# Kernel optimization log

Hardware: AMD Instinct MI355X
Metric: run time of the kernel (lower is better)

Reference implementation:

```python
import jax, jax.numpy as jnp
import numpy as np

N, T, D, H = 32, 2048, 512, 512

def setup_inputs() -> dict:
    key = jax.random.key(0)
    k1, k2, k3, k4 = jax.random.split(key, 4)
    x = jax.random.normal(k1, (N, T, D), dtype=jnp.float32)
    h0 = jax.random.normal(k2, (N, H), dtype=jnp.float32)
    Wx = jax.random.normal(k3, (D, 4 * H), dtype=jnp.float32) / np.sqrt(D)
    Wh = jax.random.normal(k4, (H, 4 * H), dtype=jnp.float32) / np.sqrt(H)
    b = jnp.zeros((4 * H,), dtype=jnp.float32)
    return {"x": x, "h0": h0, "Wx": Wx, "Wh": Wh, "b": b}

def reference(x, h0, Wx, Wh, b):
    # Precompute input contributions for all timesteps: (N, T, 4H)
    xWx = jnp.einsum('ntd,dk->ntk', x, Wx) + b
    c0 = jnp.zeros_like(h0)
    Hd = h0.shape[-1]

    def step(carry, a_x):
        prev_h, prev_c = carry
        a = a_x + prev_h @ Wh  # (N, 4H)
        i = jax.nn.sigmoid(a[:, 0 * Hd:1 * Hd])
        f = jax.nn.sigmoid(a[:, 1 * Hd:2 * Hd])
        o = jax.nn.sigmoid(a[:, 2 * Hd:3 * Hd])
        g = jnp.tanh(a[:, 3 * Hd:4 * Hd])
        next_c = f * prev_c + i * g
        next_h = o * jnp.tanh(next_c)
        return (next_h, next_c), next_h

    # scan over time: move T to leading axis
    _, hs = jax.lax.scan(step, (h0, c0), jnp.swapaxes(xWx, 0, 1))
    return jnp.swapaxes(hs, 0, 1)  # (N, T, H)
```

## Files before the change

### kernel.cpp

```cpp
#include <hip/hip_runtime.h>

typedef __attribute__((ext_vector_type(8))) __bf16 bf16x8;
typedef __attribute__((ext_vector_type(4))) float f32x4;
typedef __attribute__((ext_vector_type(2))) float f32x2;
typedef __attribute__((ext_vector_type(4))) unsigned int u32x4;
typedef unsigned int u32;
typedef unsigned long long u64;

#define NSEQ 32
#define TTOT 2048
#define DIM  512
#define HID  512
#define G4   2048
#define NGEMM 224
#define NTILE 8192
#define LEAD  96

#define AL(p)     __hip_atomic_load((p), __ATOMIC_RELAXED, __HIP_MEMORY_SCOPE_AGENT)
#define AS(p, v)  __hip_atomic_store((p), (v), __ATOMIC_RELAXED, __HIP_MEMORY_SCOPE_AGENT)
#define AX(p, v)  __hip_atomic_exchange((p), (v), __ATOMIC_RELAXED, __HIP_MEMORY_SCOPE_AGENT)

__device__ __forceinline__ float sigmoidf_(float x) {
    return 1.0f / (1.0f + __expf(-x));
}
__device__ __forceinline__ float tanhf_(float x) {
    return 2.0f / (1.0f + __expf(-2.0f * x)) - 1.0f;
}
__device__ __forceinline__ float bflo(u32 v) { return __builtin_bit_cast(float, v << 16); }
__device__ __forceinline__ float bfhi(u32 v) { return __builtin_bit_cast(float, v & 0xffff0000u); }


__global__ void lstm_init(const float* __restrict__ Wx, const float* __restrict__ Wh,
                          const float* __restrict__ h0,
                          __bf16* __restrict__ WxbT, __bf16* __restrict__ WhbT,
                          __bf16* __restrict__ hcomm, u32* __restrict__ sent,
                          u32* __restrict__ doneT, u32* __restrict__ recT,
                          float* __restrict__ cstate)
{
    int idx = blockIdx.x * 256 + threadIdx.x;
    int c = idx & (G4 - 1);
    int k = idx >> 11;
    WxbT[(size_t)c * DIM + k] = (__bf16)Wx[idx];
    WhbT[(size_t)c * HID + k] = (__bf16)Wh[idx];
    if (idx < NSEQ * HID) {
        int seq = idx >> 9, cc = idx & 511;
        int i = seq >> 4, s = seq & 15;
        hcomm[(size_t)i * 8192 + (cc >> 5) * 512 + s * 32 + (cc & 31)] = (__bf16)h0[idx];
        cstate[idx] = 0.0f;
    }
    if (idx < 128) sent[idx] = 0;
    if (idx < 512) doneT[idx] = 0;
    if (idx < 1)   recT[idx] = 0;
}

__global__ __launch_bounds__(256, 1) void lstm_mono(
    const float* __restrict__ x,
    const __bf16* __restrict__ WxbT,
    const float* __restrict__ bvec,
    const __bf16* __restrict__ WhbT,
    __bf16* __restrict__ hcomm,
    u32* __restrict__ sent,
    u32* __restrict__ doneT,
    u32* __restrict__ recT,
    __bf16* __restrict__ AxwB,
    float* __restrict__ cstate,
    float* __restrict__ out)
{
    const int bid  = blockIdx.x;
    const int tid  = threadIdx.x;
    const int w    = tid >> 6;
    const int lane = tid & 63;
    const int l15  = lane & 15;
    const int lq   = lane >> 4;

    __shared__ float P[2][4][16][132];

    if (bid >= 32) {
        const int wm = w >> 1, wn = w & 1;
        for (int tile = bid - 32; tile < NTILE; tile += NGEMM) {
            const int ts = tile >> 4;
            const int cb = (tile & 15) * 128;
            const int m0 = ts * 128;

            {
                const int need = 4 * ts - LEAD;
                if (need > 0)
                    while ((int)AL(recT) < need) __builtin_amdgcn_s_sleep(8);
            }

            f32x4 acc[4][4] = {};
            const float* xrow[4];
#pragma unroll
            for (int mi = 0; mi < 4; ++mi) {
                int r = m0 + wm * 64 + mi * 16 + l15;
                int t = r >> 5, n = r & 31;
                xrow[mi] = x + ((size_t)n * TTOT + t) * DIM;
            }
            const __bf16* bcol[4];
#pragma unroll
            for (int ni = 0; ni < 4; ++ni)
                bcol[ni] = WxbT + (size_t)(cb + wn * 64 + ni * 16 + l15) * DIM;

            for (int k0 = 0; k0 < DIM; k0 += 32) {
                bf16x8 af[4], bfr[4];
#pragma unroll
                for (int mi = 0; mi < 4; ++mi) {
                    const float* p = xrow[mi] + k0 + lq * 8;
                    f32x4 f0 = *(const f32x4*)p;
                    f32x4 f1 = *(const f32x4*)(p + 4);
                    bf16x8 a;
                    a[0] = (__bf16)f0[0]; a[1] = (__bf16)f0[1]; a[2] = (__bf16)f0[2]; a[3] = (__bf16)f0[3];
                    a[4] = (__bf16)f1[0]; a[5] = (__bf16)f1[1]; a[6] = (__bf16)f1[2]; a[7] = (__bf16)f1[3];
                    af[mi] = a;
                }
#pragma unroll
                for (int ni = 0; ni < 4; ++ni)
                    bfr[ni] = *(const bf16x8*)(bcol[ni] + k0 + lq * 8);
#pragma unroll
                for (int mi = 0; mi < 4; ++mi)
#pragma unroll
                    for (int ni = 0; ni < 4; ++ni)
                        acc[mi][ni] = __builtin_amdgcn_mfma_f32_16x16x32_bf16(af[mi], bfr[ni], acc[mi][ni], 0, 0, 0);
            }

#pragma unroll
            for (int ni = 0; ni < 4; ++ni) {
                int col = cb + wn * 64 + ni * 16 + l15;
                float bias = bvec[col];
#pragma unroll
                for (int mi = 0; mi < 4; ++mi) {
#pragma unroll
                    for (int jj = 0; jj < 4; ++jj) {
                        int r = m0 + wm * 64 + mi * 16 + lq * 4 + jj;
                        float f = acc[mi][ni][jj] + bias;
                        u32 hb  = (u32)__builtin_bit_cast(unsigned short, (__bf16)f);
                        u32 p01 = hb | ((u32)__shfl_xor((int)hb, 1) << 16);
                        u32 p23 = (u32)__shfl_xor((int)p01, 2);
                        if ((l15 & 3) == 0) {
                            u64 pk = (u64)p01 | ((u64)p23 << 32);
                            AS((u64*)AxwB + (((size_t)r * G4 + col) >> 2), pk);
                        }
                    }
                }
            }
            __syncthreads();
            if (tid == 0)
                __hip_atomic_fetch_add(&doneT[ts], 1u, __ATOMIC_RELAXED, __HIP_MEMORY_SCOPE_AGENT);
        }
        return;
    }

    const int i = bid >> 4;
    const int j = bid & 15;

    bf16x8 bfrag[8][4];
#pragma unroll
    for (int n = 0; n < 8; ++n) {
        const __bf16* base = WhbT
            + (size_t)((n >> 1) * 512 + j * 32 + (n & 1) * 16 + l15) * HID
            + (4 * w) * 32 + lq * 8;
#pragma unroll
        for (int kk = 0; kk < 4; ++kk)
            bfrag[n][kk] = *(const bf16x8*)(base + kk * 32);
    }
#pragma unroll
    for (int n = 0; n < 8; ++n)
#pragma unroll
        for (int kk = 0; kk < 4; ++kk)
            asm volatile("" : "+v"(bfrag[n][kk]));

    const int s   = tid >> 4;
    const int cp  = tid & 15;
    const int seq = i * 16 + s;
    const int hc0 = j * 32 + 2 * cp;
    float c0 = cstate[seq * HID + hc0];
    float c1 = cstate[seq * HID + hc0 + 1];

    const u32* sw = sent + i * 64 + 16 * w;
    int ok_t = -1;
    u32 pv = 0; int pv_ok = 0;

    for (int t = 0; t < TTOT; ++t) {
        if (t > ok_t) {
            u32 dv;
            do { dv = AL(&doneT[t >> 2]); } while (dv < 16u);
            ok_t = t | 3;
            pv_ok = 0;
            asm volatile("" ::: "memory");
        }

        const size_t arow = (size_t)(t * 32 + seq) * G4 + hc0;
        u32 a0 = AL((const u32*)(AxwB + arow));
        u32 a1 = AL((const u32*)(AxwB + arow + 512));
        u32 a2 = AL((const u32*)(AxwB + arow + 1024));
        u32 a3 = AL((const u32*)(AxwB + arow + 1536));

        {
            int v0 = (int)AL(&sw[l15]);
            int v1 = (int)AL(&sw[l15]);
            int v2 = (int)AL(&sw[l15]);
            int v3 = (int)AL(&sw[l15]);
            while (!__all(v0 >= t)) {
                v0 = v1; v1 = v2; v2 = v3;
                v3 = (int)AL(&sw[l15]);
            }
        }
        asm volatile("" ::: "memory");
        __builtin_amdgcn_sched_barrier(0);

        const u64* slotr = (const u64*)hcomm + (size_t)(t & 7) * 4096 + (size_t)i * 2048;
        u64 d[4][2];
#pragma unroll
        for (int kk = 0; kk < 4; ++kk) {
            const u64* p = slotr + (size_t)(4 * w + kk) * 128 + l15 * 8 + lq * 2;
            d[kk][0] = AL(p);
            d[kk][1] = AL(p + 1);
        }

        f32x4 acc[8] = {};
#pragma unroll
        for (int kk = 0; kk < 4; ++kk) {
            u32x4 q = { (u32)d[kk][0], (u32)(d[kk][0] >> 32),
                        (u32)d[kk][1], (u32)(d[kk][1] >> 32) };
            bf16x8 a = __builtin_bit_cast(bf16x8, q);
#pragma unroll
            for (int n = 0; n < 8; ++n)
                acc[n] = __builtin_amdgcn_mfma_f32_16x16x32_bf16(a, bfrag[n][kk], acc[n], 0, 0, 0);
        }

        const int par = t & 1;
#pragma unroll
        for (int n = 0; n < 8; ++n)
#pragma unroll
            for (int jj = 0; jj < 4; ++jj)
                P[par][w][lq * 4 + jj][n * 16 + l15] = acc[n][jj];
        __syncthreads();

        f32x2 sq[4];
#pragma unroll
        for (int q = 0; q < 4; ++q) {
            f32x2 v0 = *(const f32x2*)&P[par][0][s][q * 32 + 2 * cp];
            f32x2 v1 = *(const f32x2*)&P[par][1][s][q * 32 + 2 * cp];
            f32x2 v2 = *(const f32x2*)&P[par][2][s][q * 32 + 2 * cp];
            f32x2 v3 = *(const f32x2*)&P[par][3][s][q * 32 + 2 * cp];
            sq[q].x = (v0.x + v1.x) + (v2.x + v3.x);
            sq[q].y = (v0.y + v1.y) + (v2.y + v3.y);
        }

        float i0 = sigmoidf_(sq[0].x + bflo(a0)), f0 = sigmoidf_(sq[1].x + bflo(a1));
        float o0 = sigmoidf_(sq[2].x + bflo(a2)), g0 = tanhf_(sq[3].x + bflo(a3));
        c0 = f0 * c0 + i0 * g0;
        float h0v = o0 * tanhf_(c0);
        float i1 = sigmoidf_(sq[0].y + bfhi(a0)), f1 = sigmoidf_(sq[1].y + bfhi(a1));
        float o1 = sigmoidf_(sq[2].y + bfhi(a2)), g1 = tanhf_(sq[3].y + bfhi(a3));
        c1 = f1 * c1 + i1 * g1;
        float h1v = o1 * tanhf_(c1);

        {
            u32 v01 = (u32)__builtin_bit_cast(unsigned short, (__bf16)h0v)
                    | ((u32)__builtin_bit_cast(unsigned short, (__bf16)h1v) << 16);
            u32 prt = (u32)__shfl_xor((int)v01, 1);
            if (!(cp & 1)) {
                u64 pk = (u64)v01 | ((u64)prt << 32);
                AS((u64*)hcomm + (size_t)((t + 1) & 7) * 4096
                       + (size_t)i * 2048 + (size_t)j * 128 + s * 8 + (cp >> 1), pk);
            }
        }
        asm volatile("s_waitcnt vmcnt(0)" ::: "memory");
        if (lane == 0)
            AX(&sent[i * 64 + j * 4 + w], (u32)(t + 1));
        if (bid == 0 && tid == 0)
            AX(recT, (u32)(t + 1));

        *(f32x2*)(out + ((size_t)seq * TTOT + t) * HID + hc0) = (f32x2){h0v, h1v};

        if (pv_ok && pv >= 16u) ok_t += 4;
        {
            int ns = (ok_t + 1) >> 2;
            if (ns < 512) { pv = AL(&doneT[ns]); pv_ok = 1; }
            else pv_ok = 0;
        }
    }

    cstate[seq * HID + hc0]     = c0;
    cstate[seq * HID + hc0 + 1] = c1;
}

extern "C" void kernel_launch(void* const* d_in, const int* in_sizes, int n_in,
                              void* d_out, int out_size, void* d_ws, size_t ws_size,
                              hipStream_t stream)
{
    const float* x  = (const float*)d_in[0];
    const float* h0 = (const float*)d_in[1];
    const float* Wx = (const float*)d_in[2];
    const float* Wh = (const float*)d_in[3];
    const float* b  = (const float*)d_in[4];
    float* out = (float*)d_out;

    char* ws = (char*)d_ws;
    __bf16* WxbT   = (__bf16*)(ws);
    __bf16* WhbT   = (__bf16*)(ws + (2u << 20));
    __bf16* hcomm  = (__bf16*)(ws + (4u << 20));
    u32*    sent   = (u32*)(ws + (4u << 20) + (256u << 10));
    u32*    doneT  = (u32*)(ws + (4u << 20) + (257u << 10));
    u32*    recT   = (u32*)(ws + (4u << 20) + (259u << 10));
    float*  cstate = (float*)(ws + (4u << 20) + (260u << 10));
    __bf16* AxwB   = (__bf16*)(ws + (4u << 20) + (512u << 10));

    lstm_init<<<dim3((G4 * DIM) / 256), dim3(256), 0, stream>>>(
        Wx, Wh, h0, WxbT, WhbT, hcomm, sent, doneT, recT, cstate);

    lstm_mono<<<dim3(256), dim3(256), 0, stream>>>(
        x, WxbT, b, WhbT, hcomm, sent, doneT, recT, AxwB, cstate, out);
}
```

Baseline: 6.534 ms.

## Replace per-step sent flags with tagged hidden-state words for inter-block sync

Hidden-state exchange now packs each bf16 value with a 16-bit timestep tag in a 32-bit word, so consumers poll the data itself instead of waiting on separate sent counters. This removes the vmcnt(0) wait, the atomic exchange on flags, and one round-trip of flag polling per step in the serial recurrence. In exchange the communication buffer doubles in size, consumers must unpack tags, and a whole wave spins until every fragment carries the expected tag. Relaxed stores of 64-bit words rely on per-word atomicity for correctness.

```diff
diff --git a/kernel.cpp b/kernel.cpp
--- a/kernel.cpp
+++ b/kernel.cpp
@@ -15,6 +15,7 @@
 #define NGEMM 224
 #define NTILE 8192
 #define LEAD  96
+#define TAGM 0x0000ffff0000ffffull
 
 #define AL(p)     __hip_atomic_load((p), __ATOMIC_RELAXED, __HIP_MEMORY_SCOPE_AGENT)
 #define AS(p, v)  __hip_atomic_store((p), (v), __ATOMIC_RELAXED, __HIP_MEMORY_SCOPE_AGENT)
@@ -33,22 +34,30 @@
 __global__ void lstm_init(const float* __restrict__ Wx, const float* __restrict__ Wh,
                           const float* __restrict__ h0,
                           __bf16* __restrict__ WxbT, __bf16* __restrict__ WhbT,
-                          __bf16* __restrict__ hcomm, u32* __restrict__ sent,
-                          u32* __restrict__ doneT, u32* __restrict__ recT,
-                          float* __restrict__ cstate)
+                          u32* __restrict__ hctag, u32* __restrict__ doneT,
+                          u32* __restrict__ recT, float* __restrict__ cstate)
 {
     int idx = blockIdx.x * 256 + threadIdx.x;
     int c = idx & (G4 - 1);
     int k = idx >> 11;
     WxbT[(size_t)c * DIM + k] = (__bf16)Wx[idx];
     WhbT[(size_t)c * HID + k] = (__bf16)Wh[idx];
-    if (idx < NSEQ * HID) {
-        int seq = idx >> 9, cc = idx & 511;
-        int i = seq >> 4, s = seq & 15;
-        hcomm[(size_t)i * 8192 + (cc >> 5) * 512 + s * 32 + (cc & 31)] = (__bf16)h0[idx];
-        cstate[idx] = 0.0f;
+    if (idx < 131072) {
+        u32 v = 0;
+        if (idx < 16384) {
+            int f  = idx >> 1;
+            int i  = f >> 12;
+            int j  = (f >> 8) & 15;
+            int s  = (f >> 4) & 15;
+            int cp = f & 15;
+            int seq = i * 16 + s;
+            int col = j * 32 + cp * 2 + (idx & 1);
+            __bf16 hb = (__bf16)h0[seq * HID + col];
+            v = ((u32)__builtin_bit_cast(unsigned short, hb) << 16) | 1u;
+        }
+        hctag[idx] = v;
     }
-    if (idx < 128) sent[idx] = 0;
+    if (idx < NSEQ * HID) cstate[idx] = 0.0f;
     if (idx < 512) doneT[idx] = 0;
     if (idx < 1)   recT[idx] = 0;
 }
@@ -58,8 +67,7 @@
     const __bf16* __restrict__ WxbT,
     const float* __restrict__ bvec,
     const __bf16* __restrict__ WhbT,
-    __bf16* __restrict__ hcomm,
-    u32* __restrict__ sent,
+    u32* __restrict__ hctag,
     u32* __restrict__ doneT,
     u32* __restrict__ recT,
     __bf16* __restrict__ AxwB,
@@ -176,7 +184,6 @@
     float c0 = cstate[seq * HID + hc0];
     float c1 = cstate[seq * HID + hc0 + 1];
 
-    const u32* sw = sent + i * 64 + 16 * w;
     int ok_t = -1;
     u32 pv = 0; int pv_ok = 0;
 
@@ -195,34 +202,42 @@
         u32 a2 = AL((const u32*)(AxwB + arow + 1024));
         u32 a3 = AL((const u32*)(AxwB + arow + 1536));
 
-        {
-            int v0 = (int)AL(&sw[l15]);
-            int v1 = (int)AL(&sw[l15]);
-            int v2 = (int)AL(&sw[l15]);
-            int v3 = (int)AL(&sw[l15]);
-            while (!__all(v0 >= t)) {
-                v0 = v1; v1 = v2; v2 = v3;
-                v3 = (int)AL(&sw[l15]);
-            }
-        }
-        asm volatile("" ::: "memory");
+        const u64* hbase = (const u64*)hctag + (size_t)(t & 7) * 8192 + (size_t)i * 4096;
+        const u32 etag = (u32)(t + 1);
+        const u64 pat  = (u64)etag | ((u64)etag << 32);
+
+        u64 va[4][4];
+#pragma unroll
+        for (int kk = 0; kk < 4; ++kk) {
+            const u64* p = hbase + (size_t)(4 * w + kk) * 256 + l15 * 16 + lq * 4;
+#pragma unroll
+            for (int e = 0; e < 4; ++e)
+                va[kk][e] = AL(p + e);
+        }
         __builtin_amdgcn_sched_barrier(0);
 
-        const u64* slotr = (const u64*)hcomm + (size_t)(t & 7) * 4096 + (size_t)i * 2048;
-        u64 d[4][2];
+        f32x4 acc[8] = {};
 #pragma unroll
         for (int kk = 0; kk < 4; ++kk) {
-            const u64* p = slotr + (size_t)(4 * w + kk) * 128 + l15 * 8 + lq * 2;
-            d[kk][0] = AL(p);
-            d[kk][1] = AL(p + 1);
-        }
-
-        f32x4 acc[8] = {};
-#pragma unroll
-        for (int kk = 0; kk < 4; ++kk) {
-            u32x4 q = { (u32)d[kk][0], (u32)(d[kk][0] >> 32),
-                        (u32)d[kk][1], (u32)(d[kk][1] >> 32) };
-            bf16x8 a = __builtin_bit_cast(bf16x8, q);
+            const u64* p = hbase + (size_t)(4 * w + kk) * 256 + l15 * 16 + lq * 4;
+            bool ok = (((va[kk][0] ^ pat) & TAGM) == 0ull) &&
+                      (((va[kk][1] ^ pat) & TAGM) == 0ull) &&
+                      (((va[kk][2] ^ pat) & TAGM) == 0ull) &&
+                      (((va[kk][3] ^ pat) & TAGM) == 0ull);
+            while (!__all(ok)) {
+#pragma unroll
+                for (int e = 0; e < 4; ++e)
+                    va[kk][e] = AL(p + e);
+                ok = (((va[kk][0] ^ pat) & TAGM) == 0ull) &&
+                     (((va[kk][1] ^ pat) & TAGM) == 0ull) &&
+                     (((va[kk][2] ^ pat) & TAGM) == 0ull) &&
+                     (((va[kk][3] ^ pat) & TAGM) == 0ull);
+            }
+            u32 q0 = ((u32)(va[kk][0] >> 16) & 0xffffu) | ((u32)(va[kk][0] >> 32) & 0xffff0000u);
+            u32 q1 = ((u32)(va[kk][1] >> 16) & 0xffffu) | ((u32)(va[kk][1] >> 32) & 0xffff0000u);
+            u32 q2 = ((u32)(va[kk][2] >> 16) & 0xffffu) | ((u32)(va[kk][2] >> 32) & 0xffff0000u);
+            u32 q3 = ((u32)(va[kk][3] >> 16) & 0xffffu) | ((u32)(va[kk][3] >> 32) & 0xffff0000u);
+            bf16x8 a = __builtin_bit_cast(bf16x8, (u32x4){q0, q1, q2, q3});
 #pragma unroll
             for (int n = 0; n < 8; ++n)
                 acc[n] = __builtin_amdgcn_mfma_f32_16x16x32_bf16(a, bfrag[n][kk], acc[n], 0, 0, 0);
@@ -257,18 +272,15 @@
         float h1v = o1 * tanhf_(c1);
 
         {
-            u32 v01 = (u32)__builtin_bit_cast(unsigned short, (__bf16)h0v)
-                    | ((u32)__builtin_bit_cast(unsigned short, (__bf16)h1v) << 16);
-            u32 prt = (u32)__shfl_xor((int)v01, 1);
-            if (!(cp & 1)) {
-                u64 pk = (u64)v01 | ((u64)prt << 32);
-                AS((u64*)hcomm + (size_t)((t + 1) & 7) * 4096
-                       + (size_t)i * 2048 + (size_t)j * 128 + s * 8 + (cp >> 1), pk);
-            }
-        }
-        asm volatile("s_waitcnt vmcnt(0)" ::: "memory");
-        if (lane == 0)
-            AX(&sent[i * 64 + j * 4 + w], (u32)(t + 1));
+            const u32 tg2 = (u32)(t + 2);
+            u32 w0 = ((u32)__builtin_bit_cast(unsigned short, (__bf16)h0v) << 16) | tg2;
+            u32 w1 = ((u32)__builtin_bit_cast(unsigned short, (__bf16)h1v) << 16) | tg2;
+            u64 pk = (u64)w0 | ((u64)w1 << 32);
+            AS((u64*)hctag + (size_t)((t + 1) & 7) * 8192
+                   + (size_t)i * 4096 + (size_t)j * 256 + s * 16 + cp, pk);
+        }
+        asm volatile("" ::: "memory");
+
         if (bid == 0 && tid == 0)
             AX(recT, (u32)(t + 1));
 
@@ -300,16 +312,15 @@
     char* ws = (char*)d_ws;
     __bf16* WxbT   = (__bf16*)(ws);
     __bf16* WhbT   = (__bf16*)(ws + (2u << 20));
-    __bf16* hcomm  = (__bf16*)(ws + (4u << 20));
-    u32*    sent   = (u32*)(ws + (4u << 20) + (256u << 10));
-    u32*    doneT  = (u32*)(ws + (4u << 20) + (257u << 10));
-    u32*    recT   = (u32*)(ws + (4u << 20) + (259u << 10));
-    float*  cstate = (float*)(ws + (4u << 20) + (260u << 10));
-    __bf16* AxwB   = (__bf16*)(ws + (4u << 20) + (512u << 10));
+    u32*    hctag  = (u32*)(ws + (4u << 20));
+    u32*    doneT  = (u32*)(ws + (4u << 20) + (512u << 10));
+    u32*    recT   = (u32*)(ws + (4u << 20) + (515u << 10));
+    float*  cstate = (float*)(ws + (4u << 20) + (520u << 10));
+    __bf16* AxwB   = (__bf16*)(ws + (4u << 20) + (640u << 10));
 
     lstm_init<<<dim3((G4 * DIM) / 256), dim3(256), 0, stream>>>(
-        Wx, Wh, h0, WxbT, WhbT, hcomm, sent, doneT, recT, cstate);
+        Wx, Wh, h0, WxbT, WhbT, hctag, doneT, recT, cstate);
 
     lstm_mono<<<dim3(256), dim3(256), 0, stream>>>(
-        x, WxbT, b, WhbT, hcomm, sent, doneT, recT, AxwB, cstate, out);
-}
+        x, WxbT, b, WhbT, hctag, doneT, recT, AxwB, cstate, out);
+}
```

New measurement: 8.140 ms. +24.6%, slower.
